# Performance work log

Hardware: AMD Instinct MI355X
Metric: run time of the kernel (lower is better)

Reference implementation:

```python
import jax, jax.numpy as jnp
import numpy as np

N, E, D, L = 100000, 640000, 128, 3
EPS = 1e-5


def setup_inputs() -> dict:
    key = jax.random.key(0)
    ks = jax.random.split(key, 12)
    s = 1.0 / np.sqrt(D)
    return {
        "x": jax.random.normal(ks[0], (N, D), dtype=jnp.float32),
        "edge_index": jax.random.randint(ks[1], (2, E), 0, N, dtype=jnp.int64),
        "conv_w": jax.random.normal(ks[2], (L, D, D), dtype=jnp.float32) * s,
        "conv_b": jnp.zeros((L, D), dtype=jnp.float32),
        "gn_weight": jnp.ones((L, D), dtype=jnp.float32),
        "gn_bias": jnp.zeros((L, D), dtype=jnp.float32),
        "gn_mean_scale": jnp.ones((L, D), dtype=jnp.float32),
        "proj_w": jax.random.normal(ks[3], (D, D), dtype=jnp.float32) * s,
        "mlp_w": jax.random.normal(ks[4], (D, D), dtype=jnp.float32) * s,
        "mlp_b": jnp.zeros((D,), dtype=jnp.float32),
        "head_w": jax.random.normal(ks[5], (D, 1), dtype=jnp.float32) * s,
        "head_b": jnp.zeros((1,), dtype=jnp.float32),
    }


def _graph_norm(h, w, b, ms):
    # PyG GraphNorm over a single graph: subtract learnable-scaled mean, divide by std.
    mean = jnp.mean(h, axis=0)
    out = h - ms * mean
    var = jnp.mean(out * out, axis=0)
    return out / jnp.sqrt(var + EPS) * w + b


def reference(x, edge_index, conv_w, conv_b, gn_weight, gn_bias, gn_mean_scale,
              proj_w, mlp_w, mlp_b, head_w, head_b):
    n = x.shape[0]
    loop = jnp.arange(n, dtype=edge_index.dtype)
    row = jnp.concatenate([edge_index[0], loop])  # source
    col = jnp.concatenate([edge_index[1], loop])  # destination
    deg = jax.ops.segment_sum(jnp.ones_like(col, dtype=x.dtype), col, num_segments=n)
    dinv = jnp.where(deg > 0, jax.lax.rsqrt(deg), 0.0)
    norm = dinv[row] * dinv[col]  # [E+N]

    def gcn_conv(h, W, b):
        hw = h @ W                          # [N, D]
        msg = hw[row] * norm[:, None]       # gather + scale, [E+N, D]
        return jax.ops.segment_sum(msg, col, num_segments=n) + b

    h1 = x
    for i in range(L):
        residual = h1 @ proj_w if i == 0 else x  # shared_source skip
        h = gcn_conv(x, conv_w[i], conv_b[i])
        h = _graph_norm(h, gn_weight[i], gn_bias[i], gn_mean_scale[i])
        x = jax.nn.relu(h) + residual

    x = jax.nn.relu(x @ mlp_w + mlp_b)      # shared MLP (one layer for sizes [D, D])
    return x @ head_w + head_b              # task head -> [N, 1]
```

## Files before the change

kernel.cpp:

```cpp
#include <hip/hip_runtime.h>

#define FD 128

typedef __attribute__((ext_vector_type(8))) short bf16x8;
typedef __attribute__((ext_vector_type(4))) float f32x4;

__device__ __forceinline__ unsigned short f2bf(float f) {
  unsigned int u = __float_as_uint(f);
  unsigned int r = (u + 0x7fffu + ((u >> 16) & 1u)) >> 16;
  return (unsigned short)r;
}
__device__ __forceinline__ float bf_lo(unsigned int u) { return __uint_as_float(u << 16); }
__device__ __forceinline__ float bf_hi(unsigned int u) { return __uint_as_float(u & 0xffff0000u); }
__device__ __forceinline__ unsigned int pack_bf2(float a, float b) {
  return (unsigned int)f2bf(a) | ((unsigned int)f2bf(b) << 16);
}
__device__ __forceinline__ float bf2f_us(unsigned short s) { return __uint_as_float(((unsigned int)s) << 16); }

__global__ __launch_bounds__(256) void init_kernel(int* __restrict__ deg, int* __restrict__ fill,
    float* __restrict__ stats, int n) {
  int i = blockIdx.x * 256 + threadIdx.x;
  if (i < n) { deg[i] = 1; fill[i] = 0; }
  if (i < 768) stats[i] = 0.f;
}

__global__ __launch_bounds__(256) void edge_count_kernel(const int* __restrict__ ei, int e, int* __restrict__ deg) {
  int i = blockIdx.x * 256 + threadIdx.x;
  if (i < e) atomicAdd(&deg[ei[e + i]], 1);
}

__global__ __launch_bounds__(128) void scan1_kernel(const int* __restrict__ deg, int n,
    int* __restrict__ tmp, int* __restrict__ partials, float* __restrict__ dinv) {
  __shared__ int s[128];
  int b = blockIdx.x, t = threadIdx.x;
  int i = b * 128 + t;
  int d = (i < n) ? deg[i] : 1;
  if (i < n) dinv[i] = rsqrtf((float)d);
  s[t] = (i < n) ? (d - 1) : 0;
  __syncthreads();
  for (int off = 1; off < 128; off <<= 1) {
    int u = (t >= off) ? s[t - off] : 0;
    __syncthreads();
    s[t] += u;
    __syncthreads();
  }
  if (i < n) tmp[i] = s[t];
  if (t == 127) partials[b] = s[127];
}

__global__ __launch_bounds__(1024) void scan2_kernel(int* __restrict__ partials, int nb) {
  __shared__ int s[1024];
  int t = threadIdx.x;
  s[t] = (t < nb) ? partials[t] : 0;
  __syncthreads();
  for (int off = 1; off < 1024; off <<= 1) {
    int u = (t >= off) ? s[t - off] : 0;
    __syncthreads();
    s[t] += u;
    __syncthreads();
  }
  if (t < nb) partials[t] = (t == 0) ? 0 : s[t - 1];
}

__global__ __launch_bounds__(128) void scan3_kernel(const int* __restrict__ tmp, const int* __restrict__ partials, int* __restrict__ indptr, int n) {
  int i = blockIdx.x * 128 + threadIdx.x;
  if (i < n) indptr[i + 1] = tmp[i] + partials[blockIdx.x];
  if (i == 0) indptr[0] = 0;
}

__global__ __launch_bounds__(256) void fill_kernel(const int* __restrict__ ei, int e,
    const int* __restrict__ indptr, int* __restrict__ fill, const float* __restrict__ dinv,
    int* __restrict__ csr_src, float* __restrict__ csr_norm) {
  int i = blockIdx.x * 256 + threadIdx.x;
  if (i < e) {
    int r = ei[i];
    int c = ei[e + i];
    int pos = indptr[c] + atomicAdd(&fill[c], 1);
    csr_src[pos] = r;
    csr_norm[pos] = dinv[r] * dinv[c];
  }
}

__global__ __launch_bounds__(256) void prep_w(const float* __restrict__ conv_w, const float* __restrict__ proj_w,
    const float* __restrict__ mlp_w, unsigned short* __restrict__ Wtb) {
  int idx = blockIdx.x * 256 + threadIdx.x;
  int m = idx >> 14;
  int o = idx & 16383;
  int col = o >> 7, k = o & 127;
  const float* src = (m < 3) ? (conv_w + m * 16384) : ((m == 3) ? proj_w : mlp_w);
  Wtb[idx] = f2bf(src[k * FD + col]);
}

__global__ __launch_bounds__(256) void convert_x0(const float* __restrict__ x, unsigned int* __restrict__ xb, int total2) {
  int i = blockIdx.x * blockDim.x + threadIdx.x;
  int stride = gridDim.x * blockDim.x;
  for (; i < total2; i += stride) {
    float2 v = ((const float2*)x)[i];
    xb[i] = pack_bf2(v.x, v.y);
  }
}

template<int EPI>
__global__ __launch_bounds__(256) void mfma_gemm(const unsigned short* __restrict__ Ab,
    const unsigned short* __restrict__ Wtb, void* __restrict__ Cout, int n,
    const unsigned short* __restrict__ aggb, const float* __restrict__ sv, const float* __restrict__ tv,
    const float* __restrict__ bias, const float* __restrict__ hw, const float* __restrict__ hb)
{
  __shared__ uint4 bsh[2048];
  const int tid = threadIdx.x;
  const int l = tid & 63;
  const int w = tid >> 6;
  const int row0 = blockIdx.x * 64 + w * 16;

  #pragma unroll
  for (int it = 0; it < 8; ++it) {
    int s = it * 256 + tid;
    int nf = s >> 8, kf = (s >> 6) & 3, sl = s & 63;
    int col = nf * 16 + (sl & 15);
    bsh[s] = *(const uint4*)(Wtb + col * FD + kf * 32 + (sl >> 4) * 8);
  }

  int arow = row0 + (l & 15);
  bf16x8 a[4];
  if (arow < n) {
    const uint4* ap = (const uint4*)(Ab + (size_t)arow * FD + (l >> 4) * 8);
    #pragma unroll
    for (int kf = 0; kf < 4; ++kf) { uint4 t = ap[kf * 4]; a[kf] = *(bf16x8*)&t; }
  } else {
    #pragma unroll
    for (int kf = 0; kf < 4; ++kf) a[kf] = (bf16x8)(short)0;
  }

  __syncthreads();

  f32x4 acc[8];
  #pragma unroll
  for (int nf = 0; nf < 8; ++nf) acc[nf] = (f32x4)(0.0f);

  #pragma unroll
  for (int nf = 0; nf < 8; ++nf) {
    #pragma unroll
    for (int kf = 0; kf < 4; ++kf) {
      uint4 braw = bsh[(nf * 4 + kf) * 64 + l];
      acc[nf] = __builtin_amdgcn_mfma_f32_16x16x32_bf16(a[kf], *(bf16x8*)&braw, acc[nf], 0, 0, 0);
    }
  }

  if (EPI == 2) {
    float hsum[4] = {0.f, 0.f, 0.f, 0.f};
    #pragma unroll
    for (int nf = 0; nf < 8; ++nf) {
      int col = nf * 16 + (l & 15);
      float bm = bias[col];
      float hwc = hw[col];
      #pragma unroll
      for (int i = 0; i < 4; ++i)
        hsum[i] += fmaxf(acc[nf][i] + bm, 0.f) * hwc;
    }
    #pragma unroll
    for (int i = 0; i < 4; ++i) {
      #pragma unroll
      for (int off = 1; off < 16; off <<= 1) hsum[i] += __shfl_xor(hsum[i], off);
    }
    if ((l & 15) == 0) {
      float hb0 = hb[0];
      #pragma unroll
      for (int i = 0; i < 4; ++i) {
        int r = row0 + (l >> 4) * 4 + i;
        if (r < n) ((float*)Cout)[r] = hsum[i] + hb0;
      }
    }
  } else {
    unsigned short* outp = (unsigned short*)Cout;
    #pragma unroll
    for (int nf = 0; nf < 8; ++nf) {
      int col = nf * 16 + (l & 15);
      float s = (EPI == 1) ? sv[col] : 0.f;
      float t = (EPI == 1) ? tv[col] : 0.f;
      #pragma unroll
      for (int i = 0; i < 4; ++i) {
        int r = row0 + (l >> 4) * 4 + i;
        if (r < n) {
          float v = acc[nf][i];
          if (EPI == 1) {
            float ag = bf2f_us(aggb[(size_t)r * FD + col]);
            v += fmaxf(fmaf(ag, s, t), 0.f);
          }
          outp[(size_t)r * FD + col] = f2bf(v);
        }
      }
    }
  }
}

__global__ __launch_bounds__(256) void agg_bf16(const uint2* __restrict__ hw2, uint2* __restrict__ agg2,
    const int* __restrict__ indptr, const int* __restrict__ csr_src, const float* __restrict__ csr_norm,
    const float* __restrict__ dinv, const float* __restrict__ bias,
    float* __restrict__ colsum, float* __restrict__ colsum2, int n)
{
  __shared__ float sredS[4][2][32][4];
  __shared__ float sredQ[4][2][32][4];
  const int wv = threadIdx.x >> 6;
  const int lane = threadIdx.x & 63;
  const int half = lane >> 5;
  const int l32 = lane & 31;
  const int gw = blockIdx.x * 4 + wv;
  const int nw = gridDim.x * 4;
  const float4 b4 = ((const float4*)bias)[l32];
  float sx0 = 0.f, sx1 = 0.f, sx2 = 0.f, sx3 = 0.f;
  float q0 = 0.f, q1 = 0.f, q2 = 0.f, q3 = 0.f;

  for (int c = gw * 2 + half; c < n; c += nw * 2) {
    float di = dinv[c];
    float self = di * di;
    uint2 su = hw2[(size_t)c * 32 + l32];
    float a0 = fmaf(self, bf_lo(su.x), b4.x);
    float a1 = fmaf(self, bf_hi(su.x), b4.y);
    float a2 = fmaf(self, bf_lo(su.y), b4.z);
    float a3 = fmaf(self, bf_hi(su.y), b4.w);
    int e = indptr[c], e1 = indptr[c + 1];
    for (; e + 4 <= e1; e += 4) {
      int s0 = csr_src[e], s1 = csr_src[e + 1], s2 = csr_src[e + 2], s3 = csr_src[e + 3];
      float w0 = csr_norm[e], w1 = csr_norm[e + 1], w2 = csr_norm[e + 2], w3 = csr_norm[e + 3];
      uint2 u0 = hw2[(size_t)s0 * 32 + l32];
      uint2 u1 = hw2[(size_t)s1 * 32 + l32];
      uint2 u2 = hw2[(size_t)s2 * 32 + l32];
      uint2 u3 = hw2[(size_t)s3 * 32 + l32];
      a0 = fmaf(w0, bf_lo(u0.x), a0); a1 = fmaf(w0, bf_hi(u0.x), a1);
      a2 = fmaf(w0, bf_lo(u0.y), a2); a3 = fmaf(w0, bf_hi(u0.y), a3);
      a0 = fmaf(w1, bf_lo(u1.x), a0); a1 = fmaf(w1, bf_hi(u1.x), a1);
      a2 = fmaf(w1, bf_lo(u1.y), a2); a3 = fmaf(w1, bf_hi(u1.y), a3);
      a0 = fmaf(w2, bf_lo(u2.x), a0); a1 = fmaf(w2, bf_hi(u2.x), a1);
      a2 = fmaf(w2, bf_lo(u2.y), a2); a3 = fmaf(w2, bf_hi(u2.y), a3);
      a0 = fmaf(w3, bf_lo(u3.x), a0); a1 = fmaf(w3, bf_hi(u3.x), a1);
      a2 = fmaf(w3, bf_lo(u3.y), a2); a3 = fmaf(w3, bf_hi(u3.y), a3);
    }
    for (; e < e1; ++e) {
      int s0 = csr_src[e];
      float w0 = csr_norm[e];
      uint2 u0 = hw2[(size_t)s0 * 32 + l32];
      a0 = fmaf(w0, bf_lo(u0.x), a0); a1 = fmaf(w0, bf_hi(u0.x), a1);
      a2 = fmaf(w0, bf_lo(u0.y), a2); a3 = fmaf(w0, bf_hi(u0.y), a3);
    }
    uint2 o; o.x = pack_bf2(a0, a1); o.y = pack_bf2(a2, a3);
    agg2[(size_t)c * 32 + l32] = o;
    sx0 += a0; sx1 += a1; sx2 += a2; sx3 += a3;
    q0 += a0 * a0; q1 += a1 * a1; q2 += a2 * a2; q3 += a3 * a3;
  }

  sredS[wv][half][l32][0] = sx0; sredS[wv][half][l32][1] = sx1;
  sredS[wv][half][l32][2] = sx2; sredS[wv][half][l32][3] = sx3;
  sredQ[wv][half][l32][0] = q0; sredQ[wv][half][l32][1] = q1;
  sredQ[wv][half][l32][2] = q2; sredQ[wv][half][l32][3] = q3;
  __syncthreads();
  int t = threadIdx.x;
  int which = t >> 7, cc = t & 127;
  int rl = cc >> 2, rk = cc & 3;
  float v = 0.f;
  #pragma unroll
  for (int w2 = 0; w2 < 4; ++w2)
    #pragma unroll
    for (int h = 0; h < 2; ++h)
      v += which ? sredQ[w2][h][rl][rk] : sredS[w2][h][rl][rk];
  atomicAdd(which ? &colsum2[cc] : &colsum[cc], v);
}

__global__ void finalize_stats(const float* __restrict__ colsum, const float* __restrict__ colsum2,
    const float* __restrict__ gnw, const float* __restrict__ gnb, const float* __restrict__ ms,
    float* __restrict__ sv, float* __restrict__ tv, float inv_n)
{
  int d = threadIdx.x;
  if (d < FD) {
    float mean = colsum[d] * inv_n;
    float m2 = colsum2[d] * inv_n;
    float m = ms[d];
    float var = m2 - 2.f * m * mean * mean + m * m * mean * mean;
    float s = gnw[d] * rsqrtf(var + 1e-5f);
    sv[d] = s;
    tv[d] = gnb[d] - m * mean * s;
  }
}

__global__ __launch_bounds__(256) void apply_bf16(const uint4* __restrict__ aggb, const uint4* __restrict__ resid,
    const float* __restrict__ sv, const float* __restrict__ tv, uint4* __restrict__ outb, int total16)
{
  int i = blockIdx.x * blockDim.x + threadIdx.x;
  int stride = gridDim.x * blockDim.x;
  for (; i < total16; i += stride) {
    int d16 = i & 15;
    uint4 a = aggb[i];
    uint4 r = resid[i];
    float4 s0 = ((const float4*)sv)[d16 * 2];
    float4 s1 = ((const float4*)sv)[d16 * 2 + 1];
    float4 t0 = ((const float4*)tv)[d16 * 2];
    float4 t1 = ((const float4*)tv)[d16 * 2 + 1];
    uint4 o;
    o.x = pack_bf2(fmaxf(fmaf(bf_lo(a.x), s0.x, t0.x), 0.f) + bf_lo(r.x),
                   fmaxf(fmaf(bf_hi(a.x), s0.y, t0.y), 0.f) + bf_hi(r.x));
    o.y = pack_bf2(fmaxf(fmaf(bf_lo(a.y), s0.z, t0.z), 0.f) + bf_lo(r.y),
                   fmaxf(fmaf(bf_hi(a.y), s0.w, t0.w), 0.f) + bf_hi(r.y));
    o.z = pack_bf2(fmaxf(fmaf(bf_lo(a.z), s1.x, t1.x), 0.f) + bf_lo(r.z),
                   fmaxf(fmaf(bf_hi(a.z), s1.y, t1.y), 0.f) + bf_hi(r.z));
    o.w = pack_bf2(fmaxf(fmaf(bf_lo(a.w), s1.z, t1.z), 0.f) + bf_lo(r.w),
                   fmaxf(fmaf(bf_hi(a.w), s1.w, t1.w), 0.f) + bf_hi(r.w));
    outb[i] = o;
  }
}

extern "C" void kernel_launch(void* const* d_in, const int* in_sizes, int n_in,
                              void* d_out, int out_size, void* d_ws, size_t ws_size,
                              hipStream_t stream) {
  const float* x0      = (const float*)d_in[0];
  const int* ei        = (const int*)d_in[1];
  const float* conv_w  = (const float*)d_in[2];
  const float* conv_b  = (const float*)d_in[3];
  const float* gn_w    = (const float*)d_in[4];
  const float* gn_b    = (const float*)d_in[5];
  const float* gn_ms   = (const float*)d_in[6];
  const float* proj_w  = (const float*)d_in[7];
  const float* mlp_w   = (const float*)d_in[8];
  const float* mlp_b   = (const float*)d_in[9];
  const float* head_w  = (const float*)d_in[10];
  const float* head_b  = (const float*)d_in[11];
  float* out = (float*)d_out;

  const int n = in_sizes[0] / FD;
  const int e = in_sizes[1] / 2;
  const size_t ND = (size_t)n * FD;

  unsigned short* xb0  = (unsigned short*)d_ws;
  unsigned short* xb1  = xb0 + ND;
  unsigned short* hwb  = xb1 + ND;
  unsigned short* aggb = hwb + ND;
  unsigned short* Wtb  = aggb + ND;
  float* csr_norm = (float*)(Wtb + 5 * 16384);
  float* dinv     = csr_norm + e;
  float* stats    = dinv + n;
  float* sv       = stats + 768;
  float* tv       = sv + FD;
  int* deg     = (int*)(tv + FD);
  int* fill    = deg + n;
  int* indptr  = fill + n;
  int* tmp     = indptr + (n + 1);
  int* partials= tmp + n;
  int* csr_src = partials + 1024;

  const int nb256_n = (n + 255) / 256;
  const int nb256_e = (e + 255) / 256;
  const int nb128_n = (n + 127) / 128;

  init_kernel<<<nb256_n, 256, 0, stream>>>(deg, fill, stats, n);
  edge_count_kernel<<<nb256_e, 256, 0, stream>>>(ei, e, deg);
  scan1_kernel<<<nb128_n, 128, 0, stream>>>(deg, n, tmp, partials, dinv);
  scan2_kernel<<<1, 1024, 0, stream>>>(partials, nb128_n);
  scan3_kernel<<<nb128_n, 128, 0, stream>>>(tmp, partials, indptr, n);
  fill_kernel<<<nb256_e, 256, 0, stream>>>(ei, e, indptr, fill, dinv, csr_src, csr_norm);

  prep_w<<<320, 256, 0, stream>>>(conv_w, proj_w, mlp_w, Wtb);
  convert_x0<<<2048, 256, 0, stream>>>(x0, (unsigned int*)xb0, (int)(ND / 2));

  const int gemm_grid = (n + 63) / 64;
  const float inv_n = 1.f / (float)n;
  const int total16 = (int)(ND / 8);
  const unsigned short* Wt_conv0 = Wtb;
  const unsigned short* Wt_conv1 = Wtb + 16384;
  const unsigned short* Wt_conv2 = Wtb + 2 * 16384;
  const unsigned short* Wt_proj  = Wtb + 3 * 16384;
  const unsigned short* Wt_mlp   = Wtb + 4 * 16384;

  mfma_gemm<0><<<gemm_grid, 256, 0, stream>>>(xb0, Wt_conv0, hwb, n, nullptr, nullptr, nullptr, nullptr, nullptr, nullptr);
  agg_bf16<<<2048, 256, 0, stream>>>((const uint2*)hwb, (uint2*)aggb, indptr, csr_src, csr_norm, dinv,
                                     conv_b + 0 * FD, stats + 0 * FD, stats + 384 + 0 * FD, n);
  finalize_stats<<<1, 128, 0, stream>>>(stats + 0 * FD, stats + 384 + 0 * FD, gn_w + 0 * FD, gn_b + 0 * FD, gn_ms + 0 * FD, sv, tv, inv_n);
  mfma_gemm<1><<<gemm_grid, 256, 0, stream>>>(xb0, Wt_proj, xb1, n, aggb, sv, tv, nullptr, nullptr, nullptr);

  mfma_gemm<0><<<gemm_grid, 256, 0, stream>>>(xb1, Wt_conv1, hwb, n, nullptr, nullptr, nullptr, nullptr, nullptr, nullptr);
  agg_bf16<<<2048, 256, 0, stream>>>((const uint2*)hwb, (uint2*)aggb, indptr, csr_src, csr_norm, dinv,
                                     conv_b + 1 * FD, stats + 1 * FD, stats + 384 + 1 * FD, n);
  finalize_stats<<<1, 128, 0, stream>>>(stats + 1 * FD, stats + 384 + 1 * FD, gn_w + 1 * FD, gn_b + 1 * FD, gn_ms + 1 * FD, sv, tv, inv_n);
  apply_bf16<<<2048, 256, 0, stream>>>((const uint4*)aggb, (const uint4*)xb1, sv, tv, (uint4*)xb0, total16);

  mfma_gemm<0><<<gemm_grid, 256, 0, stream>>>(xb0, Wt_conv2, hwb, n, nullptr, nullptr, nullptr, nullptr, nullptr, nullptr);
  agg_bf16<<<2048, 256, 0, stream>>>((const uint2*)hwb, (uint2*)aggb, indptr, csr_src, csr_norm, dinv,
                                     conv_b + 2 * FD, stats + 2 * FD, stats + 384 + 2 * FD, n);
  finalize_stats<<<1, 128, 0, stream>>>(stats + 2 * FD, stats + 384 + 2 * FD, gn_w + 2 * FD, gn_b + 2 * FD, gn_ms + 2 * FD, sv, tv, inv_n);
  apply_bf16<<<2048, 256, 0, stream>>>((const uint4*)aggb, (const uint4*)xb0, sv, tv, (uint4*)xb1, total16);

  mfma_gemm<2><<<gemm_grid, 256, 0, stream>>>(xb1, Wt_mlp, out, n, nullptr, nullptr, nullptr, mlp_b, head_w, head_b);
}
```

Before: 446.1 us.

## Fuse GraphNorm apply into following GEMM prologue and widen aggregation loads

Removes the standalone apply_bf16 kernels. The GraphNorm scale/shift, ReLU and residual add now run in the A-operand load of the next GEMM, which also writes the new activation when it is needed later. The final layer skips that write entirely. Separately, the aggregation kernel now processes each node with 16 lanes loading 16-byte vectors instead of 32 lanes loading 8-byte vectors, adding a 2-edge tail step. This cuts a full read/write pass over the activations per layer and raises the gather width, at the cost of extra registers in the GEMM prologue and redundant scale/shift vector loads per lane.

```diff
diff --git a/kernel.cpp b/kernel.cpp
--- a/kernel.cpp
+++ b/kernel.cpp
@@ -100,11 +100,13 @@
   }
 }
 
-template<int EPI>
+template<int EPI, bool FUSEA>
 __global__ __launch_bounds__(256) void mfma_gemm(const unsigned short* __restrict__ Ab,
     const unsigned short* __restrict__ Wtb, void* __restrict__ Cout, int n,
     const unsigned short* __restrict__ aggb, const float* __restrict__ sv, const float* __restrict__ tv,
-    const float* __restrict__ bias, const float* __restrict__ hw, const float* __restrict__ hb)
+    const float* __restrict__ bias, const float* __restrict__ hw, const float* __restrict__ hb,
+    const float* __restrict__ svA, const float* __restrict__ tvA,
+    const unsigned short* __restrict__ residA, unsigned short* __restrict__ xout)
 {
   __shared__ uint4 bsh[2048];
   const int tid = threadIdx.x;
@@ -120,12 +122,39 @@
     bsh[s] = *(const uint4*)(Wtb + col * FD + kf * 32 + (sl >> 4) * 8);
   }
 
-  int arow = row0 + (l & 15);
+  const int arow = row0 + (l & 15);
   bf16x8 a[4];
   if (arow < n) {
-    const uint4* ap = (const uint4*)(Ab + (size_t)arow * FD + (l >> 4) * 8);
-    #pragma unroll
-    for (int kf = 0; kf < 4; ++kf) { uint4 t = ap[kf * 4]; a[kf] = *(bf16x8*)&t; }
+    if (FUSEA) {
+      const uint4* agp = (const uint4*)(Ab + (size_t)arow * FD + (l >> 4) * 8);
+      const uint4* rsp = (const uint4*)(residA + (size_t)arow * FD + (l >> 4) * 8);
+      uint4* xop = xout ? (uint4*)(xout + (size_t)arow * FD + (l >> 4) * 8) : nullptr;
+      #pragma unroll
+      for (int kf = 0; kf < 4; ++kf) {
+        uint4 ag = agp[kf * 4];
+        uint4 rs = rsp[kf * 4];
+        int cb4 = kf * 8 + (l >> 4) * 2;
+        float4 s0 = ((const float4*)svA)[cb4];
+        float4 s1 = ((const float4*)svA)[cb4 + 1];
+        float4 t0 = ((const float4*)tvA)[cb4];
+        float4 t1 = ((const float4*)tvA)[cb4 + 1];
+        uint4 pk;
+        pk.x = pack_bf2(fmaxf(fmaf(bf_lo(ag.x), s0.x, t0.x), 0.f) + bf_lo(rs.x),
+                        fmaxf(fmaf(bf_hi(ag.x), s0.y, t0.y), 0.f) + bf_hi(rs.x));
+        pk.y = pack_bf2(fmaxf(fmaf(bf_lo(ag.y), s0.z, t0.z), 0.f) + bf_lo(rs.y),
+                        fmaxf(fmaf(bf_hi(ag.y), s0.w, t0.w), 0.f) + bf_hi(rs.y));
+        pk.z = pack_bf2(fmaxf(fmaf(bf_lo(ag.z), s1.x, t1.x), 0.f) + bf_lo(rs.z),
+                        fmaxf(fmaf(bf_hi(ag.z), s1.y, t1.y), 0.f) + bf_hi(rs.z));
+        pk.w = pack_bf2(fmaxf(fmaf(bf_lo(ag.w), s1.z, t1.z), 0.f) + bf_lo(rs.w),
+                        fmaxf(fmaf(bf_hi(ag.w), s1.w, t1.w), 0.f) + bf_hi(rs.w));
+        a[kf] = *(bf16x8*)&pk;
+        if (xop) xop[kf * 4] = pk;
+      }
+    } else {
+      const uint4* ap = (const uint4*)(Ab + (size_t)arow * FD + (l >> 4) * 8);
+      #pragma unroll
+      for (int kf = 0; kf < 4; ++kf) { uint4 t = ap[kf * 4]; a[kf] = *(bf16x8*)&t; }
+    }
   } else {
     #pragma unroll
     for (int kf = 0; kf < 4; ++kf) a[kf] = (bf16x8)(short)0;
@@ -193,75 +222,86 @@
   }
 }
 
-__global__ __launch_bounds__(256) void agg_bf16(const uint2* __restrict__ hw2, uint2* __restrict__ agg2,
+__device__ __forceinline__ void acc8(float* a, uint4 u, float wn) {
+  a[0] = fmaf(wn, bf_lo(u.x), a[0]); a[1] = fmaf(wn, bf_hi(u.x), a[1]);
+  a[2] = fmaf(wn, bf_lo(u.y), a[2]); a[3] = fmaf(wn, bf_hi(u.y), a[3]);
+  a[4] = fmaf(wn, bf_lo(u.z), a[4]); a[5] = fmaf(wn, bf_hi(u.z), a[5]);
+  a[6] = fmaf(wn, bf_lo(u.w), a[6]); a[7] = fmaf(wn, bf_hi(u.w), a[7]);
+}
+
+__global__ __launch_bounds__(256) void agg_bf16(const uint4* __restrict__ hw4, uint4* __restrict__ agg4,
     const int* __restrict__ indptr, const int* __restrict__ csr_src, const float* __restrict__ csr_norm,
     const float* __restrict__ dinv, const float* __restrict__ bias,
     float* __restrict__ colsum, float* __restrict__ colsum2, int n)
 {
-  __shared__ float sredS[4][2][32][4];
-  __shared__ float sredQ[4][2][32][4];
+  __shared__ float sredS[4][4][16][8];
+  __shared__ float sredQ[4][4][16][8];
   const int wv = threadIdx.x >> 6;
   const int lane = threadIdx.x & 63;
-  const int half = lane >> 5;
-  const int l32 = lane & 31;
-  const int gw = blockIdx.x * 4 + wv;
-  const int nw = gridDim.x * 4;
-  const float4 b4 = ((const float4*)bias)[l32];
-  float sx0 = 0.f, sx1 = 0.f, sx2 = 0.f, sx3 = 0.f;
-  float q0 = 0.f, q1 = 0.f, q2 = 0.f, q3 = 0.f;
-
-  for (int c = gw * 2 + half; c < n; c += nw * 2) {
+  const int q = lane >> 4;
+  const int l16 = lane & 15;
+  const int gs = blockIdx.x * 16 + wv * 4 + q;
+  const int ns = gridDim.x * 16;
+  const float4 b0 = ((const float4*)bias)[l16 * 2];
+  const float4 b1 = ((const float4*)bias)[l16 * 2 + 1];
+  float st[8], sq[8];
+  #pragma unroll
+  for (int j = 0; j < 8; ++j) { st[j] = 0.f; sq[j] = 0.f; }
+
+  for (int c = gs; c < n; c += ns) {
     float di = dinv[c];
     float self = di * di;
-    uint2 su = hw2[(size_t)c * 32 + l32];
-    float a0 = fmaf(self, bf_lo(su.x), b4.x);
-    float a1 = fmaf(self, bf_hi(su.x), b4.y);
-    float a2 = fmaf(self, bf_lo(su.y), b4.z);
-    float a3 = fmaf(self, bf_hi(su.y), b4.w);
-    int e = indptr[c], e1 = indptr[c + 1];
+    uint4 su = hw4[(size_t)c * 16 + l16];
+    float a[8];
+    a[0] = fmaf(self, bf_lo(su.x), b0.x); a[1] = fmaf(self, bf_hi(su.x), b0.y);
+    a[2] = fmaf(self, bf_lo(su.y), b0.z); a[3] = fmaf(self, bf_hi(su.y), b0.w);
+    a[4] = fmaf(self, bf_lo(su.z), b1.x); a[5] = fmaf(self, bf_hi(su.z), b1.y);
+    a[6] = fmaf(self, bf_lo(su.w), b1.z); a[7] = fmaf(self, bf_hi(su.w), b1.w);
+    int e = indptr[c];
+    const int e1 = indptr[c + 1];
     for (; e + 4 <= e1; e += 4) {
       int s0 = csr_src[e], s1 = csr_src[e + 1], s2 = csr_src[e + 2], s3 = csr_src[e + 3];
       float w0 = csr_norm[e], w1 = csr_norm[e + 1], w2 = csr_norm[e + 2], w3 = csr_norm[e + 3];
-      uint2 u0 = hw2[(size_t)s0 * 32 + l32];
-      uint2 u1 = hw2[(size_t)s1 * 32 + l32];
-      uint2 u2 = hw2[(size_t)s2 * 32 + l32];
-      uint2 u3 = hw2[(size_t)s3 * 32 + l32];
-      a0 = fmaf(w0, bf_lo(u0.x), a0); a1 = fmaf(w0, bf_hi(u0.x), a1);
-      a2 = fmaf(w0, bf_lo(u0.y), a2); a3 = fmaf(w0, bf_hi(u0.y), a3);
-      a0 = fmaf(w1, bf_lo(u1.x), a0); a1 = fmaf(w1, bf_hi(u1.x), a1);
-      a2 = fmaf(w1, bf_lo(u1.y), a2); a3 = fmaf(w1, bf_hi(u1.y), a3);
-      a0 = fmaf(w2, bf_lo(u2.x), a0); a1 = fmaf(w2, bf_hi(u2.x), a1);
-      a2 = fmaf(w2, bf_lo(u2.y), a2); a3 = fmaf(w2, bf_hi(u2.y), a3);
-      a0 = fmaf(w3, bf_lo(u3.x), a0); a1 = fmaf(w3, bf_hi(u3.x), a1);
-      a2 = fmaf(w3, bf_lo(u3.y), a2); a3 = fmaf(w3, bf_hi(u3.y), a3);
-    }
-    for (; e < e1; ++e) {
+      uint4 u0 = hw4[(size_t)s0 * 16 + l16];
+      uint4 u1 = hw4[(size_t)s1 * 16 + l16];
+      uint4 u2 = hw4[(size_t)s2 * 16 + l16];
+      uint4 u3 = hw4[(size_t)s3 * 16 + l16];
+      acc8(a, u0, w0); acc8(a, u1, w1); acc8(a, u2, w2); acc8(a, u3, w3);
+    }
+    if (e + 2 <= e1) {
+      int s0 = csr_src[e], s1 = csr_src[e + 1];
+      float w0 = csr_norm[e], w1 = csr_norm[e + 1];
+      uint4 u0 = hw4[(size_t)s0 * 16 + l16];
+      uint4 u1 = hw4[(size_t)s1 * 16 + l16];
+      acc8(a, u0, w0); acc8(a, u1, w1);
+      e += 2;
+    }
+    if (e < e1) {
       int s0 = csr_src[e];
       float w0 = csr_norm[e];
-      uint2 u0 = hw2[(size_t)s0 * 32 + l32];
-      a0 = fmaf(w0, bf_lo(u0.x), a0); a1 = fmaf(w0, bf_hi(u0.x), a1);
-      a2 = fmaf(w0, bf_lo(u0.y), a2); a3 = fmaf(w0, bf_hi(u0.y), a3);
-    }
-    uint2 o; o.x = pack_bf2(a0, a1); o.y = pack_bf2(a2, a3);
-    agg2[(size_t)c * 32 + l32] = o;
-    sx0 += a0; sx1 += a1; sx2 += a2; sx3 += a3;
-    q0 += a0 * a0; q1 += a1 * a1; q2 += a2 * a2; q3 += a3 * a3;
-  }
-
-  sredS[wv][half][l32][0] = sx0; sredS[wv][half][l32][1] = sx1;
-  sredS[wv][half][l32][2] = sx2; sredS[wv][half][l32][3] = sx3;
-  sredQ[wv][half][l32][0] = q0; sredQ[wv][half][l32][1] = q1;
-  sredQ[wv][half][l32][2] = q2; sredQ[wv][half][l32][3] = q3;
+      uint4 u0 = hw4[(size_t)s0 * 16 + l16];
+      acc8(a, u0, w0);
+    }
+    uint4 o;
+    o.x = pack_bf2(a[0], a[1]); o.y = pack_bf2(a[2], a[3]);
+    o.z = pack_bf2(a[4], a[5]); o.w = pack_bf2(a[6], a[7]);
+    agg4[(size_t)c * 16 + l16] = o;
+    #pragma unroll
+    for (int j = 0; j < 8; ++j) { st[j] += a[j]; sq[j] += a[j] * a[j]; }
+  }
+
+  #pragma unroll
+  for (int j = 0; j < 8; ++j) { sredS[wv][q][l16][j] = st[j]; sredQ[wv][q][l16][j] = sq[j]; }
   __syncthreads();
   int t = threadIdx.x;
   int which = t >> 7, cc = t & 127;
-  int rl = cc >> 2, rk = cc & 3;
+  int rl = cc >> 3, rk = cc & 7;
   float v = 0.f;
   #pragma unroll
   for (int w2 = 0; w2 < 4; ++w2)
     #pragma unroll
-    for (int h = 0; h < 2; ++h)
-      v += which ? sredQ[w2][h][rl][rk] : sredS[w2][h][rl][rk];
+    for (int q2 = 0; q2 < 4; ++q2)
+      v += which ? sredQ[w2][q2][rl][rk] : sredS[w2][q2][rl][rk];
   atomicAdd(which ? &colsum2[cc] : &colsum[cc], v);
 }
 
@@ -278,32 +318,6 @@
     float s = gnw[d] * rsqrtf(var + 1e-5f);
     sv[d] = s;
     tv[d] = gnb[d] - m * mean * s;
-  }
-}
-
-__global__ __launch_bounds__(256) void apply_bf16(const uint4* __restrict__ aggb, const uint4* __restrict__ resid,
-    const float* __restrict__ sv, const float* __restrict__ tv, uint4* __restrict__ outb, int total16)
-{
-  int i = blockIdx.x * blockDim.x + threadIdx.x;
-  int stride = gridDim.x * blockDim.x;
-  for (; i < total16; i += stride) {
-    int d16 = i & 15;
-    uint4 a = aggb[i];
-    uint4 r = resid[i];
-    float4 s0 = ((const float4*)sv)[d16 * 2];
-    float4 s1 = ((const float4*)sv)[d16 * 2 + 1];
-    float4 t0 = ((const float4*)tv)[d16 * 2];
-    float4 t1 = ((const float4*)tv)[d16 * 2 + 1];
-    uint4 o;
-    o.x = pack_bf2(fmaxf(fmaf(bf_lo(a.x), s0.x, t0.x), 0.f) + bf_lo(r.x),
-                   fmaxf(fmaf(bf_hi(a.x), s0.y, t0.y), 0.f) + bf_hi(r.x));
-    o.y = pack_bf2(fmaxf(fmaf(bf_lo(a.y), s0.z, t0.z), 0.f) + bf_lo(r.y),
-                   fmaxf(fmaf(bf_hi(a.y), s0.w, t0.w), 0.f) + bf_hi(r.y));
-    o.z = pack_bf2(fmaxf(fmaf(bf_lo(a.z), s1.x, t1.x), 0.f) + bf_lo(r.z),
-                   fmaxf(fmaf(bf_hi(a.z), s1.y, t1.y), 0.f) + bf_hi(r.z));
-    o.w = pack_bf2(fmaxf(fmaf(bf_lo(a.w), s1.z, t1.z), 0.f) + bf_lo(r.w),
-                   fmaxf(fmaf(bf_hi(a.w), s1.w, t1.w), 0.f) + bf_hi(r.w));
-    outb[i] = o;
   }
 }
 
@@ -361,30 +375,35 @@
 
   const int gemm_grid = (n + 63) / 64;
   const float inv_n = 1.f / (float)n;
-  const int total16 = (int)(ND / 8);
   const unsigned short* Wt_conv0 = Wtb;
   const unsigned short* Wt_conv1 = Wtb + 16384;
   const unsigned short* Wt_conv2 = Wtb + 2 * 16384;
   const unsigned short* Wt_proj  = Wtb + 3 * 16384;
   const unsigned short* Wt_mlp   = Wtb + 4 * 16384;
 
-  mfma_gemm<0><<<gemm_grid, 256, 0, stream>>>(xb0, Wt_conv0, hwb, n, nullptr, nullptr, nullptr, nullptr, nullptr, nullptr);
-  agg_bf16<<<2048, 256, 0, stream>>>((const uint2*)hwb, (uint2*)aggb, indptr, csr_src, csr_norm, dinv,
+  mfma_gemm<0, false><<<gemm_grid, 256, 0, stream>>>(xb0, Wt_conv0, hwb, n,
+      nullptr, nullptr, nullptr, nullptr, nullptr, nullptr, nullptr, nullptr, nullptr, nullptr);
+  agg_bf16<<<2048, 256, 0, stream>>>((const uint4*)hwb, (uint4*)aggb, indptr, csr_src, csr_norm, dinv,
                                      conv_b + 0 * FD, stats + 0 * FD, stats + 384 + 0 * FD, n);
-  finalize_stats<<<1, 128, 0, stream>>>(stats + 0 * FD, stats + 384 + 0 * FD, gn_w + 0 * FD, gn_b + 0 * FD, gn_ms + 0 * FD, sv, tv, inv_n);
-  mfma_gemm<1><<<gemm_grid, 256, 0, stream>>>(xb0, Wt_proj, xb1, n, aggb, sv, tv, nullptr, nullptr, nullptr);
-
-  mfma_gemm<0><<<gemm_grid, 256, 0, stream>>>(xb1, Wt_conv1, hwb, n, nullptr, nullptr, nullptr, nullptr, nullptr, nullptr);
-  agg_bf16<<<2048, 256, 0, stream>>>((const uint2*)hwb, (uint2*)aggb, indptr, csr_src, csr_norm, dinv,
+  finalize_stats<<<1, 128, 0, stream>>>(stats + 0 * FD, stats + 384 + 0 * FD,
+      gn_w + 0 * FD, gn_b + 0 * FD, gn_ms + 0 * FD, sv, tv, inv_n);
+  mfma_gemm<1, false><<<gemm_grid, 256, 0, stream>>>(xb0, Wt_proj, xb1, n,
+      aggb, sv, tv, nullptr, nullptr, nullptr, nullptr, nullptr, nullptr, nullptr);
+
+  mfma_gemm<0, false><<<gemm_grid, 256, 0, stream>>>(xb1, Wt_conv1, hwb, n,
+      nullptr, nullptr, nullptr, nullptr, nullptr, nullptr, nullptr, nullptr, nullptr, nullptr);
+  agg_bf16<<<2048, 256, 0, stream>>>((const uint4*)hwb, (uint4*)aggb, indptr, csr_src, csr_norm, dinv,
                                      conv_b + 1 * FD, stats + 1 * FD, stats + 384 + 1 * FD, n);
-  finalize_stats<<<1, 128, 0, stream>>>(stats + 1 * FD, stats + 384 + 1 * FD, gn_w + 1 * FD, gn_b + 1 * FD, gn_ms + 1 * FD, sv, tv, inv_n);
-  apply_bf16<<<2048, 256, 0, stream>>>((const uint4*)aggb, (const uint4*)xb1, sv, tv, (uint4*)xb0, total16);
-
-  mfma_gemm<0><<<gemm_grid, 256, 0, stream>>>(xb0, Wt_conv2, hwb, n, nullptr, nullptr, nullptr, nullptr, nullptr, nullptr);
-  agg_bf16<<<2048, 256, 0, stream>>>((const uint2*)hwb, (uint2*)aggb, indptr, csr_src, csr_norm, dinv,
+  finalize_stats<<<1, 128, 0, stream>>>(stats + 1 * FD, stats + 384 + 1 * FD,
+      gn_w + 1 * FD, gn_b + 1 * FD, gn_ms + 1 * FD, sv, tv, inv_n);
+
+  mfma_gemm<0, true><<<gemm_grid, 256, 0, stream>>>(aggb, Wt_conv2, hwb, n,
+      nullptr, nullptr, nullptr, nullptr, nullptr, nullptr, sv, tv, xb1, xb0);
+  agg_bf16<<<2048, 256, 0, stream>>>((const uint4*)hwb, (uint4*)aggb, indptr, csr_src, csr_norm, dinv,
                                      conv_b + 2 * FD, stats + 2 * FD, stats + 384 + 2 * FD, n);
-  finalize_stats<<<1, 128, 0, stream>>>(stats + 2 * FD, stats + 384 + 2 * FD, gn_w + 2 * FD, gn_b + 2 * FD, gn_ms + 2 * FD, sv, tv, inv_n);
-  apply_bf16<<<2048, 256, 0, stream>>>((const uint4*)aggb, (const uint4*)xb0, sv, tv, (uint4*)xb1, total16);
-
-  mfma_gemm<2><<<gemm_grid, 256, 0, stream>>>(xb1, Wt_mlp, out, n, nullptr, nullptr, nullptr, mlp_b, head_w, head_b);
-}
+  finalize_stats<<<1, 128, 0, stream>>>(stats + 2 * FD, stats + 384 + 2 * FD,
+      gn_w + 2 * FD, gn_b + 2 * FD, gn_ms + 2 * FD, sv, tv, inv_n);
+
+  mfma_gemm<2, true><<<gemm_grid, 256, 0, stream>>>(aggb, Wt_mlp, out, n,
+      nullptr, nullptr, nullptr, mlp_b, head_w, head_b, sv, tv, xb0, nullptr);
+}
```

Result: faster. 419.7 us (-5.9%).
